# Kernel tuning notes

Measured on AMD Instinct MI355X. Metric: run time of the kernel, lower is better.

## Reference

```python
import jax, jax.numpy as jnp
import numpy as np

B, E, S, H, HD, M, MLP = 8, 1024, 2000, 16, 64, 10, 4096
EPS = 1e-5

def setup_inputs() -> dict:
    key = jax.random.key(0)
    ks = jax.random.split(key, 12)
    s = lambda k, shape, sc: jax.random.normal(k, shape, dtype=jnp.float32) * sc
    return {
        'X': s(ks[0], (B, E, S), 1.0),
        'Wq': s(ks[1], (H, HD, E), E ** -0.5), 'bq': s(ks[2], (H, HD), 0.02),
        'Wk': s(ks[3], (H, HD, E), E ** -0.5), 'bk': s(ks[4], (H, HD), 0.02),
        'Wv': s(ks[5], (H, HD, E), E ** -0.5), 'bv': s(ks[6], (H, HD), 0.02),
        'g1': jnp.ones((E,), jnp.float32), 'be1': jnp.zeros((E,), jnp.float32),
        'W1': s(ks[7], (MLP, E), E ** -0.5), 'b1': s(ks[8], (MLP,), 0.02),
        'W2': s(ks[9], (E, MLP), MLP ** -0.5), 'b2': s(ks[10], (E,), 0.02),
        'g2': jnp.ones((E,), jnp.float32), 'be2': jnp.zeros((E,), jnp.float32),
    }

def iterative_inv(K, n_iter=6):
    I = jnp.eye(K.shape[-1], dtype=K.dtype)
    # global (over all batch/head) max row-sum * max col-sum init, as in Nystromformer
    V = K.swapaxes(-1, -2) / (jnp.max(jnp.sum(jnp.abs(K), axis=-2)) * jnp.max(jnp.sum(jnp.abs(K), axis=-1)))
    for _ in range(n_iter):
        KV = K @ V
        V = 0.25 * V @ (13.0 * I - KV @ (15.0 * I - KV @ (7.0 * I - KV)))
    return V

def layer_norm(x, g, b):
    mu = jnp.mean(x, axis=-1, keepdims=True)
    var = jnp.var(x, axis=-1, keepdims=True)
    return (x - mu) * jax.lax.rsqrt(var + EPS) * g + b

def reference(X, Wq, bq, Wk, bk, Wv, bv, g1, be1, W1, b1, W2, b2, g2, be2):
    x = jnp.swapaxes(X, 1, 2)  # (B, S, E)
    # per-head projections (stacked): (B, H, S, HD)
    Q = jnp.einsum('bse,hde->bhsd', x, Wq) + bq[None, :, None, :]
    K = jnp.einsum('bse,hde->bhsd', x, Wk) + bk[None, :, None, :]
    V = jnp.einsum('bse,hde->bhsd', x, Wv) + bv[None, :, None, :]
    scale = 1.0 / np.sqrt(np.sqrt(HD)).astype(np.float32)
    Q = Q * scale
    K = K * scale
    # landmarks: mean over segments of length S//M -> (B, H, M, HD)
    Ql = Q.reshape(B, H, M, S // M, HD).mean(axis=-2)
    Kl = K.reshape(B, H, M, S // M, HD).mean(axis=-2)
    k1 = jax.nn.softmax(jnp.einsum('bhsd,bhmd->bhsm', Q, Kl), axis=-1)   # (B,H,S,M)
    k2 = jax.nn.softmax(jnp.einsum('bhnd,bhmd->bhnm', Ql, Kl), axis=-1)  # (B,H,M,M)
    k3 = jax.nn.softmax(jnp.einsum('bhmd,bhsd->bhms', Ql, K), axis=-1)   # (B,H,M,S)
    attn = (k1 @ iterative_inv(k2)) @ (k3 @ V)  # (B,H,S,HD)
    attn = jnp.swapaxes(attn, 1, 2).reshape(B, S, E)
    h = layer_norm(attn, g1, be1)
    h = jax.nn.gelu(h @ W1.T + b1, approximate=False)
    h = h @ W2.T + b2
    h = layer_norm(h, g2, be2)
    return jnp.swapaxes(h, 2, 1)  # (B, E, S)
```

## Files before the change

kernel.cpp:

```cpp
#include <hip/hip_runtime.h>
#include <cmath>
#include <cstdint>
#include <cstddef>

#define BB 8
#define EE 1024
#define SS 2000
#define HH 16
#define HDIM 64
#define MLM 10
#define MLPD 4096
#define QKV_N 3072
#define MPAD 16384
#define QK_SCALE 0.35355339059327373f

typedef __attribute__((ext_vector_type(8))) short short8v;
typedef __attribute__((ext_vector_type(4))) float f32x4;

static __device__ __forceinline__ short f2bf(float x) {
  unsigned u = __builtin_bit_cast(unsigned, x);
  unsigned r = (u + 0x7fffu + ((u >> 16) & 1u)) >> 16;
  return (short)(unsigned short)r;
}
static __device__ __forceinline__ float bf2f(short x) {
  unsigned u = ((unsigned)(unsigned short)x) << 16;
  return __builtin_bit_cast(float, u);
}

static __device__ __forceinline__ float gelu_f(float v) {
  float x = v * 0.70710678118f;
  float ax = fabsf(x);
  float t = 1.f / (1.f + 0.3275911f * ax);
  float poly = t * (0.254829592f + t * (-0.284496736f + t * (1.421413741f +
               t * (-1.453152027f + t * 1.061405429f))));
  float e = __expf(-ax * ax);
  float erf_ax = 1.f - poly * e;
  float er = (x < 0.f) ? -erf_ax : erf_ax;
  return 0.5f * v * (1.f + er);
}

static __device__ __forceinline__ void load_lds16(const short* g, short* l) {
  __builtin_amdgcn_global_load_lds(
      (const __attribute__((address_space(1))) void*)g,
      (__attribute__((address_space(3))) void*)l, 16, 0, 0);
}

__global__ __launch_bounds__(256) void transpose_x(const float* __restrict__ X, short* __restrict__ xb) {
  __shared__ float tile[32][33];
  int b = blockIdx.z;
  int e0 = blockIdx.y * 32;
  int s0 = blockIdx.x * 32;
  int tx = threadIdx.x;
  int ty = threadIdx.y;
#pragma unroll
  for (int i = 0; i < 32; i += 8) {
    int e = e0 + ty + i, s = s0 + tx;
    tile[ty + i][tx] = (s < SS) ? X[((size_t)b * EE + e) * SS + s] : 0.f;
  }
  __syncthreads();
#pragma unroll
  for (int i = 0; i < 32; i += 8) {
    int s = s0 + ty + i, e = e0 + tx;
    if (s < SS) xb[((size_t)b * SS + s) * EE + e] = f2bf(tile[tx][ty + i]);
  }
}

__global__ __launch_bounds__(256) void cast_f2b(const float* __restrict__ src, short* __restrict__ dst, int n) {
  int i = blockIdx.x * 256 + threadIdx.x;
  int stride = gridDim.x * 256;
  for (; i < n; i += stride) dst[i] = f2bf(src[i]);
}

__global__ __launch_bounds__(512, 2) void gemm256(
    const short* __restrict__ A, const short* __restrict__ Bm, void* __restrict__ Cv,
    int K, int N, int mode, int Mstore,
    const float* __restrict__ p0, const float* __restrict__ p1, const float* __restrict__ p2)
{
  __shared__ __align__(16) short lds[65536];
  const int tid = threadIdx.x;

  const int xcd = blockIdx.x & 7;
  const int idx = blockIdx.x >> 3;
  const int m0 = (((xcd << 3) | (idx & 7))) << 8;
  const int n0 = (idx >> 3) << 8;

  const int lane = tid & 63, wv = tid >> 6;
  const int wm = wv >> 2, wn = wv & 3;
  const int lm = lane & 15, quad = lane >> 4;
  const int swz = ((lm >> 3) & 1) << 1;
  const int aoff = (wm * 128 + lm) * 32 + ((quad ^ swz) << 3);
  const int boff = (wn * 64  + lm) * 32 + ((quad ^ swz) << 3);

  const int srow = tid >> 2;
  const int ssl  = ((tid & 3) ^ (((tid >> 5) & 1) << 1)) << 3;
  const short* Ag = A + (size_t)(m0 + srow) * K + ssl;
  const short* Bg = Bm + (size_t)(n0 + srow) * K + ssl;
  const int wofs = wv << 9;

  f32x4 acc[8][4];
#pragma unroll
  for (int i = 0; i < 8; i++)
#pragma unroll
    for (int j = 0; j < 4; j++) acc[i][j] = (f32x4){0.f, 0.f, 0.f, 0.f};
  short8v afr0[8], bfr0[4], afr1[8], bfr1[4];

#define RGN(buf, op, kh) (&lds[((((buf)*2 + (op)) * 2 + (kh)) << 13)])
#define STG(op, buf, kh, kt) do {                                          \
    const short* gp_ = ((op) ? Bg : Ag) + ((kt) * 64 + (kh) * 32);         \
    short* lp_ = RGN(buf, op, kh) + wofs;                                  \
    load_lds16(gp_, lp_);                                                  \
    load_lds16(gp_ + (size_t)128 * K, lp_ + 4096);                         \
  } while (0)
#define STGALL(buf, kt) do {                                               \
    STG(0, buf, 0, kt); STG(1, buf, 0, kt);                                \
    STG(0, buf, 1, kt); STG(1, buf, 1, kt);                                \
  } while (0)
#define LDSET(S, buf, kh) do {                                             \
    const short* ra_ = RGN(buf, 0, kh) + aoff;                             \
    const short* rb_ = RGN(buf, 1, kh) + boff;                             \
    _Pragma("unroll") for (int i_ = 0; i_ < 8; ++i_)                       \
      afr##S[i_] = *(const short8v*)(ra_ + i_ * 512);                      \
    _Pragma("unroll") for (int j_ = 0; j_ < 4; ++j_)                       \
      bfr##S[j_] = *(const short8v*)(rb_ + j_ * 512);                      \
  } while (0)
#define MMS(S) do {                                                        \
    __builtin_amdgcn_s_setprio(1);                                         \
    _Pragma("unroll") for (int i_ = 0; i_ < 8; ++i_)                       \
      _Pragma("unroll") for (int j_ = 0; j_ < 4; ++j_)                     \
        acc[i_][j_] = __builtin_amdgcn_mfma_f32_16x16x32_bf16(             \
            afr##S[i_], bfr##S[j_], acc[i_][j_], 0, 0, 0);                 \
    __builtin_amdgcn_s_setprio(0);                                         \
  } while (0)
#define SBAR() asm volatile("s_barrier" ::: "memory")
#define WAITV(n) asm volatile("s_waitcnt vmcnt(" #n ")" ::: "memory")
#define WAITL(n) asm volatile("s_waitcnt lgkmcnt(" #n ")" ::: "memory")

#define KTILE(buf, tt, t2, NT) do {                                        \
    LDSET(1, buf, 1);                      \
    MMS(0);                                                                \
    WAITL(0);                        \
    SBAR();                                             \
    if ((t2) < (NT)) STGALL(buf, t2);    \
    MMS(1);                                \
    if ((t2) < (NT)) { WAITV(8); } else { WAITV(0); }                      \
    SBAR();                            \
  } while (0)

  const int NT = K >> 6;
  STGALL(0, 0); STGALL(1, 1);
  WAITV(8);
  SBAR();
  LDSET(0, 0, 0);

  for (int t = 0; t < NT; t += 2) {
    KTILE(0, t, t + 2, NT);
    LDSET(0, 1, 0);
    KTILE(1, t + 1, t + 3, NT);
    if (t + 2 < NT) LDSET(0, 0, 0);
  }

  const int crow0 = m0 + wm * 128 + quad * 4;
  const int ccol0 = n0 + wn * 64 + lm;
#pragma unroll
  for (int j = 0; j < 4; ++j) {
    const int col = ccol0 + j * 16;
    float bias, scl = 1.f;
    if (mode == 0) {
      if (col < 1024)      { bias = p0[col];        scl = QK_SCALE; }
      else if (col < 2048) { bias = p1[col - 1024]; scl = QK_SCALE; }
      else                 { bias = p2[col - 2048]; }
    } else {
      bias = p0[col];
    }
#pragma unroll
    for (int i = 0; i < 8; ++i) {
#pragma unroll
      for (int r = 0; r < 4; ++r) {
        const int row = crow0 + i * 16 + r;
        if (row < Mstore) {
          float v = acc[i][j][r] + bias;
          if (mode == 0)      v *= scl;
          else if (mode == 1) v = gelu_f(v);
          if (mode == 2) ((float*)Cv)[(size_t)row * N + col] = v;
          else           ((short*)Cv)[(size_t)row * N + col] = f2bf(v);
        }
      }
    }
  }
#undef RGN
#undef STG
#undef STGALL
#undef LDSET
#undef MMS
#undef SBAR
#undef WAITV
#undef WAITL
#undef KTILE
}

__global__ __launch_bounds__(64) void landmarks(const short* __restrict__ QKV, float* __restrict__ Ql, float* __restrict__ Kl) {
  int d = threadIdx.x;
  int bhm = blockIdx.x;
  int part = blockIdx.y;
  int b = bhm / (HH * MLM);
  int h = (bhm / MLM) % HH;
  int m = bhm % MLM;
  const short* src = QKV + (part ? 1024 : 0);
  size_t base = ((size_t)(b * SS + m * 200)) * QKV_N + h * HDIM + d;
  float acc = 0.f;
  for (int i = 0; i < 200; i++) acc += bf2f(src[base + (size_t)i * QKV_N]);
  float* dst = part ? Kl : Ql;
  dst[((size_t)(b * HH + h) * MLM + m) * HDIM + d] = acc * (1.f / 200.f);
}

__global__ __launch_bounds__(128) void k2stats(const float* __restrict__ Ql, const float* __restrict__ Kl,
                                               float* __restrict__ k2, float* __restrict__ cmax, float* __restrict__ rmax) {
  int bh = blockIdx.x;
  __shared__ float QlS[640], KlS[640], zz[100], k2s[100], cs[10], rs[10];
  for (int i = threadIdx.x; i < 640; i += 128) {
    QlS[i] = Ql[(size_t)bh * 640 + i];
    KlS[i] = Kl[(size_t)bh * 640 + i];
  }
  __syncthreads();
  if (threadIdx.x < 100) {
    int i = threadIdx.x / 10, j = threadIdx.x % 10;
    float z = 0.f;
    for (int d = 0; d < 64; d++) z += QlS[i * 64 + d] * KlS[j * 64 + d];
    zz[threadIdx.x] = z;
  }
  __syncthreads();
  if (threadIdx.x < 10) {
    int i = threadIdx.x;
    float mx = -1e30f;
    for (int j = 0; j < 10; j++) mx = fmaxf(mx, zz[i * 10 + j]);
    float s = 0.f, e[10];
    for (int j = 0; j < 10; j++) { e[j] = expf(zz[i * 10 + j] - mx); s += e[j]; }
    float inv = 1.f / s, rsum = 0.f;
    for (int j = 0; j < 10; j++) {
      float v = e[j] * inv;
      k2s[i * 10 + j] = v;
      k2[(size_t)bh * 100 + i * 10 + j] = v;
      rsum += v;
    }
    rs[i] = rsum;
  }
  __syncthreads();
  if (threadIdx.x < 10) {
    int j = threadIdx.x;
    float c = 0.f;
    for (int i = 0; i < 10; i++) c += k2s[i * 10 + j];
    cs[j] = c;
  }
  __syncthreads();
  if (threadIdx.x == 0) {
    float m1 = 0.f, m2 = 0.f;
    for (int j = 0; j < 10; j++) { m1 = fmaxf(m1, cs[j]); m2 = fmaxf(m2, rs[j]); }
    cmax[bh] = m1;
    rmax[bh] = m2;
  }
}

__global__ __launch_bounds__(128) void invk(const float* __restrict__ k2, const float* __restrict__ cmax,
                                            const float* __restrict__ rmax, float* __restrict__ invo) {
  int bh = blockIdx.x;
  __shared__ float gsc;
  __shared__ float Km[100], Vm[100], KV[100], Ta[100], Tb[100];
  if (threadIdx.x == 0) {
    float mc = 0.f, mr = 0.f;
    for (int i = 0; i < 128; i++) { mc = fmaxf(mc, cmax[i]); mr = fmaxf(mr, rmax[i]); }
    gsc = 1.f / (mc * mr);
  }
  for (int i = threadIdx.x; i < 100; i += 128) Km[i] = k2[(size_t)bh * 100 + i];
  __syncthreads();
  int t = threadIdx.x;
  int i = t / 10, j = t % 10;
  bool act = t < 100;
  if (act) Vm[t] = Km[j * 10 + i] * gsc;
  __syncthreads();
  for (int it = 0; it < 6; it++) {
    if (act) { float a = 0.f; for (int k = 0; k < 10; k++) a += Km[i * 10 + k] * Vm[k * 10 + j]; KV[t] = a; }
    __syncthreads();
    if (act) Ta[t] = (i == j ? 7.f : 0.f) - KV[t];
    __syncthreads();
    if (act) { float a = 0.f; for (int k = 0; k < 10; k++) a += KV[i * 10 + k] * Ta[k * 10 + j]; Tb[t] = (i == j ? 15.f : 0.f) - a; }
    __syncthreads();
    if (act) { float a = 0.f; for (int k = 0; k < 10; k++) a += KV[i * 10 + k] * Tb[k * 10 + j]; Ta[t] = (i == j ? 13.f : 0.f) - a; }
    __syncthreads();
    if (act) { float a = 0.f; for (int k = 0; k < 10; k++) a += Vm[i * 10 + k] * Ta[k * 10 + j]; Tb[t] = 0.25f * a; }
    __syncthreads();
    if (act) Vm[t] = Tb[t];
    __syncthreads();
  }
  if (act) invo[(size_t)bh * 100 + t] = Vm[t];
}

__global__ __launch_bounds__(256) void k1inv_kernel(const short* __restrict__ QKV, const float* __restrict__ Kl,
                                                    const float* __restrict__ invg, float* __restrict__ k1inv) {
  int b = blockIdx.y;
  int s0 = blockIdx.x * 16;
  __shared__ float KlS[16 * 650];
  __shared__ float invS[16 * 101];
  for (int idx = threadIdx.x; idx < 16 * 640; idx += 256) {
    int h = idx / 640, r = idx % 640;
    KlS[h * 650 + r] = Kl[(size_t)(b * HH + h) * 640 + r];
  }
  for (int idx = threadIdx.x; idx < 1600; idx += 256) {
    int h = idx / 100, r = idx % 100;
    invS[h * 101 + r] = invg[(size_t)(b * HH + h) * 100 + r];
  }
  __syncthreads();
  int sl = threadIdx.x >> 4, h = threadIdx.x & 15;
  int s = s0 + sl;
  size_t qoff = (size_t)(b * SS + s) * QKV_N + h * HDIM;
  float z[10];
#pragma unroll
  for (int m = 0; m < 10; m++) z[m] = 0.f;
  for (int c = 0; c < 8; c++) {
    short8v qv = *(const short8v*)&QKV[qoff + c * 8];
    float qf[8];
#pragma unroll
    for (int jj = 0; jj < 8; jj++) qf[jj] = bf2f(qv[jj]);
#pragma unroll
    for (int m = 0; m < 10; m++) {
      const float* kl = &KlS[h * 650 + m * 64 + c * 8];
      float a = 0.f;
#pragma unroll
      for (int jj = 0; jj < 8; jj++) a += qf[jj] * kl[jj];
      z[m] += a;
    }
  }
  float mx = z[0];
#pragma unroll
  for (int m = 1; m < 10; m++) mx = fmaxf(mx, z[m]);
  float p[10], ssum = 0.f;
#pragma unroll
  for (int m = 0; m < 10; m++) { p[m] = expf(z[m] - mx); ssum += p[m]; }
  float rinv = 1.f / ssum;
  float* dst = &k1inv[((size_t)(b * SS + s) * HH + h) * MLM];
#pragma unroll
  for (int mm = 0; mm < 10; mm++) {
    float a = 0.f;
#pragma unroll
    for (int jjj = 0; jjj < 10; jjj++) a += p[jjj] * invS[h * 101 + jjj * 10 + mm];
    dst[mm] = a * rinv;
  }
}

__global__ __launch_bounds__(256) void k3v_kernel(const short* __restrict__ QKV, const float* __restrict__ Qlg,
                                                  float* __restrict__ kvout) {
  int bh = blockIdx.x;
  int b = bh >> 4, h = bh & 15;
  __shared__ float Kt[64 * 65];
  __shared__ float Vt[64 * 65];
  __shared__ float eS[10 * 64];
  __shared__ float QlS[640];
  __shared__ float denS[10];
  int tid = threadIdx.x;
  int wave = tid >> 6, lane = tid & 63;
  for (int i = tid; i < 640; i += 256) QlS[i] = Qlg[(size_t)bh * 640 + i];
  float myden = 0.f;
  float accn[3] = {0.f, 0.f, 0.f};
  int rowi = tid >> 2;
  int d0 = (tid & 3) * 16;
  for (int s0 = 0; s0 < SS; s0 += 64) {
    __syncthreads();
    if (s0 + rowi < SS) {
      size_t base = (size_t)(b * SS + s0 + rowi) * QKV_N + h * HDIM + d0;
      short8v k0v = *(const short8v*)&QKV[base + 1024];
      short8v k1v = *(const short8v*)&QKV[base + 1024 + 8];
      short8v v0v = *(const short8v*)&QKV[base + 2048];
      short8v v1v = *(const short8v*)&QKV[base + 2048 + 8];
#pragma unroll
      for (int jj = 0; jj < 8; jj++) {
        Kt[rowi * 65 + d0 + jj]     = bf2f(k0v[jj]);
        Kt[rowi * 65 + d0 + 8 + jj] = bf2f(k1v[jj]);
        Vt[rowi * 65 + d0 + jj]     = bf2f(v0v[jj]);
        Vt[rowi * 65 + d0 + 8 + jj] = bf2f(v1v[jj]);
      }
    }
    __syncthreads();
    for (int mb = 0; mb < 12; mb += 4) {
      int m = mb + wave;
      if (m < 10) {
        float z = 0.f;
        const float* kr = &Kt[lane * 65];
        const float* ql = &QlS[m * 64];
        for (int d = 0; d < 64; d++) z += ql[d] * kr[d];
        eS[m * 64 + lane] = (s0 + lane < SS) ? expf(z) : 0.f;
      }
    }
    __syncthreads();
    if (tid < 10) {
      float a = 0.f;
      for (int slj = 0; slj < 64; slj++) a += eS[tid * 64 + slj];
      myden += a;
    }
#pragma unroll
    for (int ii = 0; ii < 3; ii++) {
      int idx = tid + ii * 256;
      if (idx < 640) {
        int m = idx >> 6, d = idx & 63;
        float a = 0.f;
        for (int slj = 0; slj < 64; slj++) a += eS[m * 64 + slj] * Vt[slj * 65 + d];
        accn[ii] += a;
      }
    }
  }
  if (tid < 10) denS[tid] = myden;
  __syncthreads();
#pragma unroll
  for (int ii = 0; ii < 3; ii++) {
    int idx = tid + ii * 256;
    if (idx < 640) {
      int m = idx >> 6;
      kvout[(size_t)bh * 640 + idx] = accn[ii] / denS[m];
    }
  }
}

__global__ __launch_bounds__(256) void attn_ln1(const float* __restrict__ k1inv, const float* __restrict__ kvg,
                                                const float* __restrict__ g1, const float* __restrict__ be1,
                                                short* __restrict__ h1) {
  int blk = blockIdx.x;
  int b = blk / SS;
  __shared__ float pS[160];
  __shared__ float red[8];
  for (int i = threadIdx.x; i < 160; i += 256) pS[i] = k1inv[(size_t)blk * 160 + i];
  __syncthreads();
  float vals[4], s1 = 0.f, s2 = 0.f;
#pragma unroll
  for (int i = 0; i < 4; i++) {
    int e = threadIdx.x + i * 256;
    int h = e >> 6, d = e & 63;
    const float* kvp = &kvg[((size_t)(b * HH + h) * MLM) * HDIM + d];
    const float* pp = &pS[h * 10];
    float a = 0.f;
#pragma unroll
    for (int m = 0; m < 10; m++) a += pp[m] * kvp[m * 64];
    vals[i] = a; s1 += a; s2 += a * a;
  }
#pragma unroll
  for (int off = 32; off; off >>= 1) { s1 += __shfl_down(s1, off); s2 += __shfl_down(s2, off); }
  int wv = threadIdx.x >> 6;
  if ((threadIdx.x & 63) == 0) { red[wv] = s1; red[4 + wv] = s2; }
  __syncthreads();
  float t1 = red[0] + red[1] + red[2] + red[3];
  float t2 = red[4] + red[5] + red[6] + red[7];
  float mean = t1 * (1.f / 1024.f);
  float var = t2 * (1.f / 1024.f) - mean * mean;
  float ninv = rsqrtf(var + 1e-5f);
#pragma unroll
  for (int i = 0; i < 4; i++) {
    int e = threadIdx.x + i * 256;
    h1[(size_t)blk * EE + e] = f2bf((vals[i] - mean) * ninv * g1[e] + be1[e]);
  }
}

__global__ __launch_bounds__(256) void ln2_kernel(const float* __restrict__ h2, const float* __restrict__ g2,
                                                  const float* __restrict__ be2, short* __restrict__ h3) {
  int blk = blockIdx.x;
  __shared__ float red[8];
  float vals[4], s1 = 0.f, s2 = 0.f;
#pragma unroll
  for (int i = 0; i < 4; i++) {
    int e = threadIdx.x + i * 256;
    float a = h2[(size_t)blk * EE + e];
    vals[i] = a; s1 += a; s2 += a * a;
  }
#pragma unroll
  for (int off = 32; off; off >>= 1) { s1 += __shfl_down(s1, off); s2 += __shfl_down(s2, off); }
  int wv = threadIdx.x >> 6;
  if ((threadIdx.x & 63) == 0) { red[wv] = s1; red[4 + wv] = s2; }
  __syncthreads();
  float t1 = red[0] + red[1] + red[2] + red[3];
  float t2 = red[4] + red[5] + red[6] + red[7];
  float mean = t1 * (1.f / 1024.f);
  float var = t2 * (1.f / 1024.f) - mean * mean;
  float ninv = rsqrtf(var + 1e-5f);
#pragma unroll
  for (int i = 0; i < 4; i++) {
    int e = threadIdx.x + i * 256;
    h3[(size_t)blk * EE + e] = f2bf((vals[i] - mean) * ninv * g2[e] + be2[e]);
  }
}

__global__ __launch_bounds__(256) void transpose_out(const short* __restrict__ h3, float* __restrict__ outp) {
  __shared__ short tile[64 * 65];
  int b = blockIdx.z;
  int e0 = blockIdx.y * 64;
  int s0 = blockIdx.x * 64;
  int tx = threadIdx.x & 63;
  int ty = threadIdx.x >> 6;
#pragma unroll
  for (int i = 0; i < 16; i++) {
    int r = ty + i * 4;
    int s = s0 + r;
    if (s < SS) tile[r * 65 + tx] = h3[((size_t)b * SS + s) * EE + e0 + tx];
  }
  __syncthreads();
#pragma unroll
  for (int i = 0; i < 16; i++) {
    int c = ty + i * 4;
    int s = s0 + tx;
    if (s < SS) outp[((size_t)b * EE + e0 + c) * SS + s] = bf2f(tile[tx * 65 + c]);
  }
}

#define ALIGN_UP(x) (((x) + 255) & ~(size_t)255)
static const size_t SZ_SLOTA = (size_t)MPAD * EE * 2;
static const size_t SZ_QKV   = (size_t)MPAD * QKV_N * 2;
static const size_t SZ_MID   = (size_t)MPAD * MLPD * 2;
static const size_t SZ_WCAT  = (size_t)QKV_N * EE * 2;
static const size_t SZ_W1B   = (size_t)MLPD * EE * 2;
static const size_t SZ_W2B   = (size_t)EE * MLPD * 2;
static const size_t SZ_QL    = (size_t)BB * HH * MLM * HDIM * 4;
static const size_t SZ_K2    = (size_t)BB * HH * 100 * 4;
static const size_t SZ_ST    = 512;

extern "C" void kernel_launch(void* const* d_in, const int* in_sizes, int n_in,
                              void* d_out, int out_size, void* d_ws, size_t ws_size,
                              hipStream_t stream) {
  const float* X   = (const float*)d_in[0];
  const float* Wq  = (const float*)d_in[1];
  const float* bq  = (const float*)d_in[2];
  const float* Wk  = (const float*)d_in[3];
  const float* bk  = (const float*)d_in[4];
  const float* Wv  = (const float*)d_in[5];
  const float* bv  = (const float*)d_in[6];
  const float* g1  = (const float*)d_in[7];
  const float* be1 = (const float*)d_in[8];
  const float* W1  = (const float*)d_in[9];
  const float* b1  = (const float*)d_in[10];
  const float* W2  = (const float*)d_in[11];
  const float* b2  = (const float*)d_in[12];
  const float* g2  = (const float*)d_in[13];
  const float* be2 = (const float*)d_in[14];

  char* ws = (char*)d_ws;
  size_t off = 0;
  char* slotA = ws + off; off += ALIGN_UP(SZ_SLOTA);
  char* slotB = ws + off; off += ALIGN_UP(SZ_MID);
  char* slotD = ws + off; off += ALIGN_UP(SZ_WCAT);
  short* W1b = (short*)(ws + off); off += ALIGN_UP(SZ_W1B);
  short* W2b = (short*)(ws + off); off += ALIGN_UP(SZ_W2B);

  short* xb   = (short*)slotA;
  short* h1   = (short*)slotA;
  short* h3   = (short*)slotA;
  short* qkv  = (short*)slotB;
  short* mid  = (short*)slotB;
  float* k1ib = (float*)(slotB + ALIGN_UP(SZ_QKV));
  short* Wcat = (short*)slotD;
  size_t doff = 0;
  float* Qlm  = (float*)(slotD + doff); doff += ALIGN_UP(SZ_QL);
  float* Klm  = (float*)(slotD + doff); doff += ALIGN_UP(SZ_QL);
  float* k2b  = (float*)(slotD + doff); doff += ALIGN_UP(SZ_K2);
  float* cmaxb= (float*)(slotD + doff); doff += ALIGN_UP(SZ_ST);
  float* rmaxb= (float*)(slotD + doff); doff += ALIGN_UP(SZ_ST);
  float* invb = (float*)(slotD + doff); doff += ALIGN_UP(SZ_K2);
  float* kvb  = (float*)(slotD + doff); doff += ALIGN_UP(SZ_QL);
  float* h2c  = (float*)d_out;
  (void)ws_size; (void)in_sizes; (void)n_in; (void)out_size;

  hipMemsetAsync(slotA + (size_t)BB * SS * EE * 2, 0,
                 (size_t)(MPAD - BB * SS) * EE * 2, stream);
  transpose_x<<<dim3(63, 32, BB), dim3(32, 8), 0, stream>>>(X, xb);
  cast_f2b<<<2048, 256, 0, stream>>>(Wq, Wcat,             EE * EE);
  cast_f2b<<<2048, 256, 0, stream>>>(Wk, Wcat + EE * EE,   EE * EE);
  cast_f2b<<<2048, 256, 0, stream>>>(Wv, Wcat + 2*EE*EE,   EE * EE);
  cast_f2b<<<4096, 256, 0, stream>>>(W1, W1b, MLPD * EE);
  cast_f2b<<<4096, 256, 0, stream>>>(W2, W2b, EE * MLPD);
  gemm256<<<64 * 12, 512, 0, stream>>>(xb, Wcat, qkv, EE, QKV_N, 0, MPAD, bq, bk, bv);
  landmarks<<<dim3(BB * HH * MLM, 2), 64, 0, stream>>>(qkv, Qlm, Klm);
  k2stats<<<BB * HH, 128, 0, stream>>>(Qlm, Klm, k2b, cmaxb, rmaxb);
  invk<<<BB * HH, 128, 0, stream>>>(k2b, cmaxb, rmaxb, invb);
  k1inv_kernel<<<dim3(125, BB), 256, 0, stream>>>(qkv, Klm, invb, k1ib);
  k3v_kernel<<<BB * HH, 256, 0, stream>>>(qkv, Qlm, kvb);
  attn_ln1<<<BB * SS, 256, 0, stream>>>(k1ib, kvb, g1, be1, h1);
  gemm256<<<64 * 16, 512, 0, stream>>>(h1, W1b, mid, EE, MLPD, 1, MPAD, b1, nullptr, nullptr);
  gemm256<<<64 * 4, 512, 0, stream>>>(mid, W2b, h2c, MLPD, EE, 2, BB * SS, b2, nullptr, nullptr);
  ln2_kernel<<<BB * SS, 256, 0, stream>>>(h2c, g2, be2, h3);
  transpose_out<<<dim3(32, 16, BB), 256, 0, stream>>>(h3, (float*)d_out);
}
```

Before: 1.155 ms.

## Load GEMM A operand directly to registers, stage only B through LDS

Restructures the bf16 GEMM so each wave loads its A fragments straight from global memory into registers while only the B tile is staged in shared memory. The wave grid changes to 4x2 with 64x128 per-wave tiles, and LDS usage halves. This aims to cut LDS traffic and footprint, but adds redundant global A reads across waves and exposes global latency to the MFMA pipeline; the vmcnt wait accounting now mixes A and B loads.

New measurement: 1.452 ms. +25.7%, slower.

```diff
diff --git a/kernel.cpp b/kernel.cpp
--- a/kernel.cpp
+++ b/kernel.cpp
@@ -76,7 +76,7 @@
     int K, int N, int mode, int Mstore,
     const float* __restrict__ p0, const float* __restrict__ p1, const float* __restrict__ p2)
 {
-  __shared__ __align__(16) short lds[65536];
+  __shared__ __align__(16) short lds[32768];
   const int tid = threadIdx.x;
 
   const int xcd = blockIdx.x & 7;
@@ -85,84 +85,81 @@
   const int n0 = (idx >> 3) << 8;
 
   const int lane = tid & 63, wv = tid >> 6;
-  const int wm = wv >> 2, wn = wv & 3;
+  const int wm = wv >> 1, wn = wv & 1;
   const int lm = lane & 15, quad = lane >> 4;
   const int swz = ((lm >> 3) & 1) << 1;
-  const int aoff = (wm * 128 + lm) * 32 + ((quad ^ swz) << 3);
-  const int boff = (wn * 64  + lm) * 32 + ((quad ^ swz) << 3);
+  const int boff = (wn * 128 + lm) * 32 + ((quad ^ swz) << 3);
 
   const int srow = tid >> 2;
   const int ssl  = ((tid & 3) ^ (((tid >> 5) & 1) << 1)) << 3;
-  const short* Ag = A + (size_t)(m0 + srow) * K + ssl;
   const short* Bg = Bm + (size_t)(n0 + srow) * K + ssl;
   const int wofs = wv << 9;
 
-  f32x4 acc[8][4];
-#pragma unroll
-  for (int i = 0; i < 8; i++)
-#pragma unroll
-    for (int j = 0; j < 4; j++) acc[i][j] = (f32x4){0.f, 0.f, 0.f, 0.f};
-  short8v afr0[8], bfr0[4], afr1[8], bfr1[4];
-
-#define RGN(buf, op, kh) (&lds[((((buf)*2 + (op)) * 2 + (kh)) << 13)])
-#define STG(op, buf, kh, kt) do {                                          \
-    const short* gp_ = ((op) ? Bg : Ag) + ((kt) * 64 + (kh) * 32);         \
-    short* lp_ = RGN(buf, op, kh) + wofs;                                  \
+  const short* Aw = A + (size_t)(m0 + wm * 64 + lm) * K + quad * 8;
+
+  f32x4 acc[4][8];
+#pragma unroll
+  for (int i = 0; i < 4; i++)
+#pragma unroll
+    for (int j = 0; j < 8; j++) acc[i][j] = (f32x4){0.f, 0.f, 0.f, 0.f};
+  short8v a0[4], a1[4], bf0[8], bf1[8];
+
+#define RGNB(buf, kh) (&lds[(((buf)*2 + (kh)) << 13)])
+#define STGB1(buf, kh, kt) do {                                            \
+    const short* gp_ = Bg + ((kt) * 64 + (kh) * 32);                       \
+    short* lp_ = RGNB(buf, kh) + wofs;                                     \
     load_lds16(gp_, lp_);                                                  \
     load_lds16(gp_ + (size_t)128 * K, lp_ + 4096);                         \
   } while (0)
-#define STGALL(buf, kt) do {                                               \
-    STG(0, buf, 0, kt); STG(1, buf, 0, kt);                                \
-    STG(0, buf, 1, kt); STG(1, buf, 1, kt);                                \
+#define STGB(buf, kt) do { STGB1(buf, 0, kt); STGB1(buf, 1, kt); } while (0)
+#define APF(S, kt, kh) do {                                                \
+    _Pragma("unroll") for (int i_ = 0; i_ < 4; ++i_)                       \
+      a##S[i_] = *(const short8v*)(Aw + (size_t)i_ * 16 * K                \
+                                   + ((kt) * 64 + (kh) * 32));             \
   } while (0)
-#define LDSET(S, buf, kh) do {                                             \
-    const short* ra_ = RGN(buf, 0, kh) + aoff;                             \
-    const short* rb_ = RGN(buf, 1, kh) + boff;                             \
-    _Pragma("unroll") for (int i_ = 0; i_ < 8; ++i_)                       \
-      afr##S[i_] = *(const short8v*)(ra_ + i_ * 512);                      \
-    _Pragma("unroll") for (int j_ = 0; j_ < 4; ++j_)                       \
-      bfr##S[j_] = *(const short8v*)(rb_ + j_ * 512);                      \
+#define LDBF(S, buf, kh) do {                                              \
+    const short* r_ = RGNB(buf, kh) + boff;                                \
+    _Pragma("unroll") for (int j_ = 0; j_ < 8; ++j_)                       \
+      bf##S[j_] = *(const short8v*)(r_ + j_ * 512);                        \
   } while (0)
-#define MMS(S) do {                                                        \
+#define MMH(S) do {                                                        \
     __builtin_amdgcn_s_setprio(1);                                         \
-    _Pragma("unroll") for (int i_ = 0; i_ < 8; ++i_)                       \
-      _Pragma("unroll") for (int j_ = 0; j_ < 4; ++j_)                     \
+    _Pragma("unroll") for (int i_ = 0; i_ < 4; ++i_)                       \
+      _Pragma("unroll") for (int j_ = 0; j_ < 8; ++j_)                     \
         acc[i_][j_] = __builtin_amdgcn_mfma_f32_16x16x32_bf16(             \
-            afr##S[i_], bfr##S[j_], acc[i_][j_], 0, 0, 0);                 \
+            a##S[i_], bf##S[j_], acc[i_][j_], 0, 0, 0);                    \
     __builtin_amdgcn_s_setprio(0);                                         \
   } while (0)
 #define SBAR() asm volatile("s_barrier" ::: "memory")
 #define WAITV(n) asm volatile("s_waitcnt vmcnt(" #n ")" ::: "memory")
-#define WAITL(n) asm volatile("s_waitcnt lgkmcnt(" #n ")" ::: "memory")
-
-#define KTILE(buf, tt, t2, NT) do {                                        \
-    LDSET(1, buf, 1);                      \
-    MMS(0);                                                                \
-    WAITL(0);                        \
-    SBAR();                                             \
-    if ((t2) < (NT)) STGALL(buf, t2);    \
-    MMS(1);                                \
-    if ((t2) < (NT)) { WAITV(8); } else { WAITV(0); }                      \
-    SBAR();                            \
+
+#define TILE(buf, t) do {                                                  \
+    LDBF(0, buf, 0);                                                       \
+    APF(1, t, 1);                                                          \
+    MMH(0);                                                                \
+    LDBF(1, buf, 1);                                                       \
+    if ((t) + 1 < NT) APF(0, (t) + 1, 0);                                  \
+    MMH(1);                                                                \
+    WAITV(8);                                                              \
+    SBAR();                                                                \
+    if ((t) + 2 < NT) STGB(buf, (t) + 2);                                  \
   } while (0)
 
   const int NT = K >> 6;
-  STGALL(0, 0); STGALL(1, 1);
+  STGB(0, 0); STGB(1, 1);
+  APF(0, 0, 0);
   WAITV(8);
   SBAR();
-  LDSET(0, 0, 0);
 
   for (int t = 0; t < NT; t += 2) {
-    KTILE(0, t, t + 2, NT);
-    LDSET(0, 1, 0);
-    KTILE(1, t + 1, t + 3, NT);
-    if (t + 2 < NT) LDSET(0, 0, 0);
-  }
-
-  const int crow0 = m0 + wm * 128 + quad * 4;
-  const int ccol0 = n0 + wn * 64 + lm;
-#pragma unroll
-  for (int j = 0; j < 4; ++j) {
+    TILE(0, t);
+    TILE(1, t + 1);
+  }
+
+  const int crow0 = m0 + wm * 64 + quad * 4;
+  const int ccol0 = n0 + wn * 128 + lm;
+#pragma unroll
+  for (int j = 0; j < 8; ++j) {
     const int col = ccol0 + j * 16;
     float bias, scl = 1.f;
     if (mode == 0) {
@@ -173,7 +170,7 @@
       bias = p0[col];
     }
 #pragma unroll
-    for (int i = 0; i < 8; ++i) {
+    for (int i = 0; i < 4; ++i) {
 #pragma unroll
       for (int r = 0; r < 4; ++r) {
         const int row = crow0 + i * 16 + r;
@@ -187,15 +184,15 @@
       }
     }
   }
-#undef RGN
-#undef STG
-#undef STGALL
-#undef LDSET
-#undef MMS
+#undef RGNB
+#undef STGB1
+#undef STGB
+#undef APF
+#undef LDBF
+#undef MMH
 #undef SBAR
 #undef WAITV
-#undef WAITL
-#undef KTILE
+#undef TILE
 }
 
 __global__ __launch_bounds__(64) void landmarks(const short* __restrict__ QKV, float* __restrict__ Ql, float* __restrict__ Kl) {
```

## Simplify GEMM main loop to single-stage prefetch with full-tile waits

Applied to the files above, without the earlier changes.

Replaces the two-tile-deep, split-k-half software pipeline in the bf16 MFMA GEMM with a simpler schedule. Each k-tile now issues the global-to-LDS load for the next tile into the other buffer, loads all B fragments and then the A fragments per half, runs the MFMAs, and waits for all outstanding vector memory before a barrier. This drops the interleaving of LDS fragment reads with MFMAs and the deeper prefetch distance. The likely aim is lower register pressure and simpler control, at the cost of exposing LDS read latency and waiting on global loads every tile.

Result: faster. 1.017 ms (-11.9%).

```diff
diff --git a/kernel.cpp b/kernel.cpp
--- a/kernel.cpp
+++ b/kernel.cpp
@@ -102,7 +102,7 @@
   for (int i = 0; i < 8; i++)
 #pragma unroll
     for (int j = 0; j < 4; j++) acc[i][j] = (f32x4){0.f, 0.f, 0.f, 0.f};
-  short8v afr0[8], bfr0[4], afr1[8], bfr1[4];
+  short8v afr[8], bfr[8];
 
 #define RGN(buf, op, kh) (&lds[((((buf)*2 + (op)) * 2 + (kh)) << 13)])
 #define STG(op, buf, kh, kt) do {                                          \
@@ -111,52 +111,52 @@
     load_lds16(gp_, lp_);                                                  \
     load_lds16(gp_ + (size_t)128 * K, lp_ + 4096);                         \
   } while (0)
-#define STGALL(buf, kt) do {                                               \
+#define STAGE(buf, kt) do {                                                \
     STG(0, buf, 0, kt); STG(1, buf, 0, kt);                                \
     STG(0, buf, 1, kt); STG(1, buf, 1, kt);                                \
   } while (0)
-#define LDSET(S, buf, kh) do {                                             \
+#define LDB_ALL(buf) do {                                                  \
+    _Pragma("unroll") for (int kh_ = 0; kh_ < 2; ++kh_) {                  \
+      const short* rb_ = RGN(buf, 1, kh_) + boff;                          \
+      _Pragma("unroll") for (int j_ = 0; j_ < 4; ++j_)                     \
+        bfr[kh_ * 4 + j_] = *(const short8v*)(rb_ + j_ * 512);             \
+    }                                                                      \
+  } while (0)
+#define LDA8(buf, kh) do {                                                 \
     const short* ra_ = RGN(buf, 0, kh) + aoff;                             \
-    const short* rb_ = RGN(buf, 1, kh) + boff;                             \
     _Pragma("unroll") for (int i_ = 0; i_ < 8; ++i_)                       \
-      afr##S[i_] = *(const short8v*)(ra_ + i_ * 512);                      \
-    _Pragma("unroll") for (int j_ = 0; j_ < 4; ++j_)                       \
-      bfr##S[j_] = *(const short8v*)(rb_ + j_ * 512);                      \
+      afr[i_] = *(const short8v*)(ra_ + i_ * 512);                         \
   } while (0)
-#define MMS(S) do {                                                        \
+#define MM32(kh) do {                                                      \
     __builtin_amdgcn_s_setprio(1);                                         \
     _Pragma("unroll") for (int i_ = 0; i_ < 8; ++i_)                       \
       _Pragma("unroll") for (int j_ = 0; j_ < 4; ++j_)                     \
         acc[i_][j_] = __builtin_amdgcn_mfma_f32_16x16x32_bf16(             \
-            afr##S[i_], bfr##S[j_], acc[i_][j_], 0, 0, 0);                 \
+            afr[i_], bfr[(kh) * 4 + j_], acc[i_][j_], 0, 0, 0);            \
     __builtin_amdgcn_s_setprio(0);                                         \
   } while (0)
 #define SBAR() asm volatile("s_barrier" ::: "memory")
 #define WAITV(n) asm volatile("s_waitcnt vmcnt(" #n ")" ::: "memory")
-#define WAITL(n) asm volatile("s_waitcnt lgkmcnt(" #n ")" ::: "memory")
-
-#define KTILE(buf, tt, t2, NT) do {                                        \
-    LDSET(1, buf, 1);                      \
-    MMS(0);                                                                \
-    WAITL(0);                        \
-    SBAR();                                             \
-    if ((t2) < (NT)) STGALL(buf, t2);    \
-    MMS(1);                                \
-    if ((t2) < (NT)) { WAITV(8); } else { WAITV(0); }                      \
-    SBAR();                            \
+
+#define KTILE(buf, t) do {                                                 \
+    if ((t) + 1 < NT) STAGE(buf ^ 1, (t) + 1);                             \
+    LDB_ALL(buf);                                                          \
+    LDA8(buf, 0);                                                          \
+    MM32(0);                                                               \
+    LDA8(buf, 1);                                                          \
+    MM32(1);                                                               \
+    WAITV(0);                                                              \
+    SBAR();                                                                \
   } while (0)
 
   const int NT = K >> 6;
-  STGALL(0, 0); STGALL(1, 1);
-  WAITV(8);
+  STAGE(0, 0);
+  WAITV(0);
   SBAR();
-  LDSET(0, 0, 0);
 
   for (int t = 0; t < NT; t += 2) {
-    KTILE(0, t, t + 2, NT);
-    LDSET(0, 1, 0);
-    KTILE(1, t + 1, t + 3, NT);
-    if (t + 2 < NT) LDSET(0, 0, 0);
+    KTILE(0, t);
+    KTILE(1, t + 1);
   }
 
   const int crow0 = m0 + wm * 128 + quad * 4;
@@ -189,12 +189,12 @@
   }
 #undef RGN
 #undef STG
-#undef STGALL
-#undef LDSET
-#undef MMS
+#undef STAGE
+#undef LDB_ALL
+#undef LDA8
+#undef MM32
 #undef SBAR
 #undef WAITV
-#undef WAITL
 #undef KTILE
 }
 
```
